# Kernel tuning notes

Hardware: AMD Instinct MI355X
Metric: run time of the kernel (lower is better)

The kernel has to match this reference:

```python
import jax, jax.numpy as jnp
import numpy as np

DIM = 1024
HEADS = 16
HEAD_DIM = DIM // HEADS
MLP_HIDDEN = DIM * 4
EPS = 1e-6


def _ln(x):
    # LayerNorm without affine, eps=1e-6
    mu = jnp.mean(x, axis=-1, keepdims=True)
    var = jnp.var(x, axis=-1, keepdims=True)
    return (x - mu) / jnp.sqrt(var + EPS)


def setup_inputs() -> dict:
    key = jax.random.key(0)
    ks = jax.random.split(key, 12)
    B, N = 8, 1024
    s = lambda fan: 1.0 / np.sqrt(fan)
    return {
        "x": jax.random.normal(ks[0], (B, N, DIM), jnp.float32),
        "c": jax.random.normal(ks[1], (B, DIM), jnp.float32),
        "w_qkv": jax.random.normal(ks[2], (DIM, 3 * DIM), jnp.float32) * s(DIM),
        "b_qkv": jnp.zeros((3 * DIM,), jnp.float32),
        "w_proj": jax.random.normal(ks[3], (DIM, DIM), jnp.float32) * s(DIM),
        "b_proj": jnp.zeros((DIM,), jnp.float32),
        "w_mlp1": jax.random.normal(ks[4], (DIM, MLP_HIDDEN), jnp.float32) * s(DIM),
        "b_mlp1": jnp.zeros((MLP_HIDDEN,), jnp.float32),
        "w_mlp2": jax.random.normal(ks[5], (MLP_HIDDEN, DIM), jnp.float32) * s(MLP_HIDDEN),
        "b_mlp2": jnp.zeros((DIM,), jnp.float32),
        "w_ada": jax.random.normal(ks[6], (DIM, 6 * DIM), jnp.float32) * s(DIM),
        "b_ada": jnp.zeros((6 * DIM,), jnp.float32),
    }


def _attention(h, w_qkv, b_qkv, w_proj, b_proj):
    B, N, C = h.shape
    qkv = h @ w_qkv + b_qkv  # [B,N,3C]
    qkv = qkv.reshape(B, N, 3, HEADS, HEAD_DIM)
    q, k, v = qkv[:, :, 0], qkv[:, :, 1], qkv[:, :, 2]  # [B,N,H,Dh]
    scale = HEAD_DIM ** -0.5
    attn = jnp.einsum("bqhd,bkhd->bhqk", q, k) * scale
    attn = jax.nn.softmax(attn, axis=-1)
    o = jnp.einsum("bhqk,bkhd->bqhd", attn, v).reshape(B, N, C)
    return o @ w_proj + b_proj


def reference(x, c, w_qkv, b_qkv, w_proj, b_proj, w_mlp1, b_mlp1, w_mlp2, b_mlp2, w_ada, b_ada):
    mod = (jax.nn.silu(c) @ w_ada + b_ada)[:, None, :]  # [B,1,6D]
    g1, be1, a1, g2, be2, a2 = jnp.split(mod, 6, axis=-1)
    h = _ln(x) * (1.0 + g1) + be1
    x = x + a1 * _attention(h, w_qkv, b_qkv, w_proj, b_proj)
    h = _ln(x) * (1.0 + g2) + be2
    mlp = jax.nn.gelu(h @ w_mlp1 + b_mlp1, approximate=False) @ w_mlp2 + b_mlp2
    return x + a2 * mlp
```

## Files before the change

kernel.cpp:

```cpp
#include <hip/hip_runtime.h>
#include <hip/hip_bf16.h>

#define DIMC 1024
#define SEQ  1024
#define NB   8
#define NH   16
#define HD2  64
#define EPSV 1e-6f

typedef short short8 __attribute__((ext_vector_type(8)));
typedef float floatx4 __attribute__((ext_vector_type(4)));

#define GLOAD_LDS(g, l) \
  __builtin_amdgcn_global_load_lds((const __attribute__((address_space(1))) unsigned int*)(g), \
                                   (__attribute__((address_space(3))) unsigned int*)(l), 16, 0, 0)

__device__ __forceinline__ float bf2f(unsigned short u){
  union { float f; unsigned int i; } v; v.i = ((unsigned int)u) << 16; return v.f;
}
__device__ __forceinline__ unsigned short f2bf(float f){
  union { float f; unsigned int i; } v; v.f = f;
  unsigned int r = v.i + 0x7fffu + ((v.i >> 16) & 1u);
  return (unsigned short)(r >> 16);
}

__device__ __forceinline__ float gelu_f(float v){
  const float z  = fabsf(v) * 0.70710678f;
  const float t  = __builtin_amdgcn_rcpf(fmaf(0.3275911f, z, 1.0f));
  float p = fmaf(t, 1.061405429f, -1.453152027f);
  p = fmaf(t, p, 1.421413741f);
  p = fmaf(t, p, -0.284496736f);
  p = fmaf(t, p, 0.254829592f);
  float erfz = fmaf(-p * t, __expf(-z * z), 1.0f);
  erfz = (v < 0.0f) ? -erfz : erfz;
  return 0.5f * v * (1.0f + erfz);
}

__global__ __launch_bounds__(256)
void tcvt_kernel(const float* __restrict__ in, unsigned short* __restrict__ out, int K, int N)
{
  __shared__ float tile[32][33];
  const int n0 = blockIdx.x * 32;
  const int k0 = blockIdx.y * 32;
  const int tx = threadIdx.x & 31;
  const int ty = threadIdx.x >> 5;
#pragma unroll
  for (int i = 0; i < 4; i++)
    tile[ty + i*8][tx] = in[(size_t)(k0 + ty + i*8) * N + n0 + tx];
  __syncthreads();
#pragma unroll
  for (int i = 0; i < 4; i++)
    out[(size_t)(n0 + ty + i*8) * K + k0 + tx] = f2bf(tile[tx][ty + i*8]);
}

__global__ __launch_bounds__(256)
void ada1_kernel(const float* __restrict__ c,
                 const float* __restrict__ w_ada,
                 float* __restrict__ partial)
{
  __shared__ float cs[NB][128];
  const int chunk = blockIdx.y;
  const int col = blockIdx.x * 256 + threadIdx.x;
  const int t = threadIdx.x;
  for (int i = t; i < NB * 128; i += 256) {
    const int b = i >> 7, k = i & 127;
    const float v = c[b * DIMC + chunk * 128 + k];
    cs[b][k] = v / (1.0f + __expf(-v));
  }
  __syncthreads();
  float acc[NB];
#pragma unroll
  for (int b = 0; b < NB; b++) acc[b] = 0.0f;
#pragma unroll 8
  for (int k = 0; k < 128; k++) {
    const float wv = w_ada[(size_t)(chunk * 128 + k) * 6144 + col];
#pragma unroll
    for (int b = 0; b < NB; b++) acc[b] = fmaf(cs[b][k], wv, acc[b]);
  }
#pragma unroll
  for (int b = 0; b < NB; b++)
    partial[((size_t)chunk * NB + b) * 6144 + col] = acc[b];
}

__global__ __launch_bounds__(256)
void ada2_kernel(const float* __restrict__ partial, const float* __restrict__ b_ada,
                 float* __restrict__ mod)
{
  const int i = blockIdx.x * 256 + threadIdx.x;
  const int b = i / 6144, col = i % 6144;
  float s = b_ada[col];
#pragma unroll
  for (int ch = 0; ch < 8; ch++) s += partial[((size_t)ch * NB + b) * 6144 + col];
  mod[i] = s;
}

__global__ __launch_bounds__(256)
void ln_kernel(const float* __restrict__ xin, const float* __restrict__ mod,
               int goff, int boff, unsigned short* __restrict__ hout)
{
  const int row = blockIdx.x;
  const int bb = row >> 10;
  const int t = threadIdx.x;
  const float4 x4 = *((const float4*)(xin + (size_t)row * DIMC) + t);
  const float v0 = x4.x, v1 = x4.y, v2 = x4.z, v3 = x4.w;
  float s  = v0 + v1 + v2 + v3;
  float ss = v0*v0 + v1*v1 + v2*v2 + v3*v3;
#pragma unroll
  for (int off = 32; off > 0; off >>= 1) {
    s  += __shfl_down(s,  off, 64);
    ss += __shfl_down(ss, off, 64);
  }
  __shared__ float red[10];
  const int w = t >> 6;
  if ((t & 63) == 0) { red[w] = s; red[4 + w] = ss; }
  __syncthreads();
  if (t == 0) {
    const float S  = red[0] + red[1] + red[2] + red[3];
    const float SS = red[4] + red[5] + red[6] + red[7];
    const float mu = S * (1.0f / 1024.0f);
    red[8] = mu;
    red[9] = rsqrtf(SS * (1.0f / 1024.0f) - mu * mu + EPSV);
  }
  __syncthreads();
  const float mu = red[8], rstd = red[9];
  const float* mrow = mod + (size_t)bb * 6144;
  const int d = t * 4;
  const float h0 = (v0 - mu) * rstd * (1.0f + mrow[goff + d + 0]) + mrow[boff + d + 0];
  const float h1 = (v1 - mu) * rstd * (1.0f + mrow[goff + d + 1]) + mrow[boff + d + 1];
  const float h2 = (v2 - mu) * rstd * (1.0f + mrow[goff + d + 2]) + mrow[boff + d + 2];
  const float h3 = (v3 - mu) * rstd * (1.0f + mrow[goff + d + 3]) + mrow[boff + d + 3];
  uint2 u;
  u.x = (unsigned)f2bf(h0) | ((unsigned)f2bf(h1) << 16);
  u.y = (unsigned)f2bf(h2) | ((unsigned)f2bf(h3) << 16);
  *((uint2*)(hout + (size_t)row * DIMC + d)) = u;
}

#define MF(a, b, c) __builtin_amdgcn_mfma_f32_16x16x32_bf16(a, b, c, 0, 0, 0)
#define FENCE() asm volatile("" ::: "memory")
#define BARRIER() do { FENCE(); __builtin_amdgcn_s_barrier(); FENCE(); } while (0)

template<int MODE, int BN>
__global__ __launch_bounds__(512, 2)
void gemm256_kernel(const unsigned short* __restrict__ A,
                    const unsigned short* __restrict__ Bt,
                    const float* __restrict__ bias,
                    void* __restrict__ Cout,
                    const float* __restrict__ resid,
                    const float* __restrict__ mod,
                    int M, int N, int K)
{
  constexpr int NWN = BN / 64;
  constexpr int NWM = 8 / NWN;
  constexpr int NI  = 256 / NWM / 16;

  __shared__ unsigned short As[2][16384];
  __shared__ unsigned short Bs[2][BN * 64];

  const int mT = M >> 8;
  const int mb = mT >> 3;
  const int bid = blockIdx.x;
  const int xcd = bid & 7;
  const int local = bid >> 3;
  const int ni = local / mb;
  const int mi = xcd * mb + (local - ni * mb);
  const int m0 = mi << 8, n0 = ni * BN;

  const int tid = threadIdx.x;
  const int w = tid >> 6, lane = tid & 63;
  const int quad = lane >> 4, c16 = lane & 15;
  const int wm = w / NWN, wn = w % NWN, w2 = w << 1;

  const int aRow = (wm * (NI * 16) + c16) * 64;
  const int bRow = (wn * 64 + c16) * 64;
  const int sxz  = (c16 & 7) << 4;
  const int swz0 = ((0  + quad * 16) ^ sxz) >> 1;
  const int swz1 = ((64 + quad * 16) ^ sxz) >> 1;
#define LDA8(cc, i, SW) (*(const short8*)&As[cc][aRow + (i) * 1024 + (SW)])
#define LDB8(cc, j, SW) (*(const short8*)&Bs[cc][bRow + (j) * 1024 + (SW)])

  const int l8 = lane >> 3, lc = lane & 7;
  const int stC = ((lc ^ l8) << 3);
  const unsigned short* aSt = A  + (size_t)(m0 + w2 * 8 + l8) * K + stC;
  const unsigned short* bSt = Bt + (size_t)(n0 + w2 * 8 + l8) * K + stC;
#define STAGE_A(cc, h, kk0) do { \
  GLOAD_LDS(aSt + (size_t)((h) * 128    ) * K + (kk0), &As[cc][(h) * 8192 + w2 * 512      ]); \
  GLOAD_LDS(aSt + (size_t)((h) * 128 + 8) * K + (kk0), &As[cc][(h) * 8192 + w2 * 512 + 512]); \
} while (0)
#define STAGE_B(cc, h, kk0) do { \
  GLOAD_LDS(bSt + (size_t)((h) * 128    ) * K + (kk0), &Bs[cc][(h) * 8192 + w2 * 512      ]); \
  GLOAD_LDS(bSt + (size_t)((h) * 128 + 8) * K + (kk0), &Bs[cc][(h) * 8192 + w2 * 512 + 512]); \
} while (0)

  floatx4 acc[NI][4];
#pragma unroll
  for (int i = 0; i < NI; i++)
#pragma unroll
    for (int j = 0; j < 4; j++) acc[i][j] = (floatx4)(0.0f);

#define MMROW(i, aE, aO) do { \
  acc[i][0] = MF(aE, bF00, acc[i][0]); acc[i][0] = MF(aO, bF01, acc[i][0]); \
  acc[i][1] = MF(aE, bF10, acc[i][1]); acc[i][1] = MF(aO, bF11, acc[i][1]); \
  acc[i][2] = MF(aE, bF20, acc[i][2]); acc[i][2] = MF(aO, bF21, acc[i][2]); \
  acc[i][3] = MF(aE, bF30, acc[i][3]); acc[i][3] = MF(aO, bF31, acc[i][3]); \
} while (0)

#define PH_TAIL(i0, i1) do { \
  BARRIER(); \
  asm volatile("s_waitcnt lgkmcnt(0)" ::: "memory"); \
  __builtin_amdgcn_s_setprio(1); \
  MMROW(i0, a0, a1); \
  MMROW(i1, a2, a3); \
  __builtin_amdgcn_s_setprio(0); \
} while (0)

#define GROUP256(cc, oo, g) do { \
  const int kA_ = ((g) + 1) << 6; const int kB_ = ((g) + 2) << 6; \
  const bool dA_ = kA_ < K; const bool dB_ = kB_ < K; \
  short8 bF00 = LDB8(cc, 0, swz0), bF01 = LDB8(cc, 0, swz1); \
  short8 bF10 = LDB8(cc, 1, swz0), bF11 = LDB8(cc, 1, swz1); \
  short8 bF20 = LDB8(cc, 2, swz0), bF21 = LDB8(cc, 2, swz1); \
  short8 bF30 = LDB8(cc, 3, swz0), bF31 = LDB8(cc, 3, swz1); \
  short8 a0 = LDA8(cc, 0, swz0), a1 = LDA8(cc, 0, swz1); \
  short8 a2 = LDA8(cc, 1, swz0), a3 = LDA8(cc, 1, swz1); \
  if (dA_) STAGE_A(oo, 0, kA_); \
  PH_TAIL(0, 1); \
  BARRIER(); \
  a0 = LDA8(cc, 2, swz0); a1 = LDA8(cc, 2, swz1); \
  a2 = LDA8(cc, 3, swz0); a3 = LDA8(cc, 3, swz1); \
  if (dA_) STAGE_A(oo, 1, kA_); \
  PH_TAIL(2, 3); \
  BARRIER(); \
  a0 = LDA8(cc, 4, swz0); a1 = LDA8(cc, 4, swz1); \
  a2 = LDA8(cc, 5, swz0); a3 = LDA8(cc, 5, swz1); \
  if (dB_) STAGE_B(cc, 0, kB_); \
  PH_TAIL(4, 5); \
  BARRIER(); \
  a0 = LDA8(cc, 6, swz0); a1 = LDA8(cc, 6, swz1); \
  a2 = LDA8(cc, 7, swz0); a3 = LDA8(cc, 7, swz1); \
  if (dB_) STAGE_B(cc, 1, kB_); \
  PH_TAIL(6, 7); \
  if (dB_) { asm volatile("s_waitcnt vmcnt(4)" ::: "memory"); } \
  else     { asm volatile("s_waitcnt vmcnt(0)" ::: "memory"); } \
  BARRIER(); \
} while (0)

#define GROUP128(cc, oo, g) do { \
  const int kA_ = ((g) + 1) << 6; const int kB_ = ((g) + 2) << 6; \
  const bool dA_ = kA_ < K; const bool dB_ = kB_ < K; \
  short8 bF00 = LDB8(cc, 0, swz0), bF01 = LDB8(cc, 0, swz1); \
  short8 bF10 = LDB8(cc, 1, swz0), bF11 = LDB8(cc, 1, swz1); \
  short8 bF20 = LDB8(cc, 2, swz0), bF21 = LDB8(cc, 2, swz1); \
  short8 bF30 = LDB8(cc, 3, swz0), bF31 = LDB8(cc, 3, swz1); \
  short8 a0 = LDA8(cc, 0, swz0), a1 = LDA8(cc, 0, swz1); \
  short8 a2 = LDA8(cc, 1, swz0), a3 = LDA8(cc, 1, swz1); \
  if (dA_) { STAGE_A(oo, 0, kA_); STAGE_A(oo, 1, kA_); } \
  PH_TAIL(0, 1); \
  BARRIER(); \
  a0 = LDA8(cc, 2, swz0); a1 = LDA8(cc, 2, swz1); \
  a2 = LDA8(cc, 3, swz0); a3 = LDA8(cc, 3, swz1); \
  if (dB_) STAGE_B(cc, 0, kB_); \
  PH_TAIL(2, 3); \
  if (dB_) { asm volatile("s_waitcnt vmcnt(2)" ::: "memory"); } \
  else     { asm volatile("s_waitcnt vmcnt(0)" ::: "memory"); } \
  BARRIER(); \
} while (0)

  if constexpr (BN == 256) {
    STAGE_B(0, 0, 0);  STAGE_B(0, 1, 0);
    STAGE_A(0, 0, 0);  STAGE_A(0, 1, 0);
    STAGE_B(1, 0, 64); STAGE_B(1, 1, 64);
    asm volatile("s_waitcnt vmcnt(4)" ::: "memory");
  } else {
    STAGE_B(0, 0, 0);
    STAGE_A(0, 0, 0);  STAGE_A(0, 1, 0);
    STAGE_B(1, 0, 64);
    asm volatile("s_waitcnt vmcnt(2)" ::: "memory");
  }
  BARRIER();

  const int T = K >> 6;
  for (int g = 0; g < T; g += 2) {
    if constexpr (BN == 256) { GROUP256(0, 1, g); GROUP256(1, 0, g + 1); }
    else                     { GROUP128(0, 1, g); GROUP128(1, 0, g + 1); }
  }

  const int bb = m0 >> 10;
  if (MODE == 0 || MODE == 1) {
    unsigned short* eb;
    if constexpr (BN == 256)
      eb = (w < 4 ? (unsigned short*)As : (unsigned short*)Bs) + (w & 3) * 8192;
    else
      eb = (unsigned short*)As + w * (NI * 1024);
#pragma unroll
    for (int j = 0; j < 4; j++) {
      const int col = n0 + wn * 64 + j * 16 + c16;
      const float bv = bias[col];
#pragma unroll
      for (int i = 0; i < NI; i++)
#pragma unroll
        for (int r = 0; r < 4; r++) {
          float v = acc[i][j][r] + bv;
          if (MODE == 1) v = gelu_f(v);
          eb[(i * 16 + quad * 4 + r) * 64 + j * 16 + c16] = f2bf(v);
        }
    }
    unsigned short* cw = (unsigned short*)Cout
                       + (size_t)(m0 + wm * (NI * 16)) * N + n0 + wn * 64;
    const int seg = lane & 7;
#pragma unroll
    for (int it = 0; it < NI * 2; it++) {
      const int row = it * 8 + (lane >> 3);
      *(uint4*)(cw + (size_t)row * N + seg * 8) = *(const uint4*)&eb[row * 64 + seg * 8];
    }
  } else {
#pragma unroll
    for (int j = 0; j < 4; j++) {
      const int col = n0 + wn * 64 + j * 16 + c16;
      const float bv = bias[col];
      const float av = mod[(size_t)bb * 6144 + (MODE == 2 ? 2048 : 5120) + col];
#pragma unroll
      for (int i = 0; i < NI; i++) {
        const int rowb = m0 + wm * (NI * 16) + i * 16 + quad * 4;
#pragma unroll
        for (int r = 0; r < 4; r++) {
          const size_t idx = (size_t)(rowb + r) * N + col;
          ((float*)Cout)[idx] = fmaf(av, acc[i][j][r] + bv, resid[idx]);
        }
      }
    }
  }
#undef GROUP256
#undef GROUP128
#undef PH_TAIL
#undef MMROW
#undef STAGE_A
#undef STAGE_B
#undef LDA8
#undef LDB8
}

__global__ __launch_bounds__(256, 2)
void fattn_kernel(const unsigned short* __restrict__ qkv, unsigned short* __restrict__ o_out)
{
  __shared__ unsigned short Ks[64][72];
  __shared__ unsigned short Vt[64][72];
  __shared__ unsigned short Pt[4][32][72];

  const int blk = blockIdx.x;
  const int qt = blk & 7;
  const int h  = (blk >> 3) & 15;
  const int bb = blk >> 7;
  const int tid = threadIdx.x;
  const int w = tid >> 6;
  const int lane = tid & 63;
  const int quad = lane >> 4;
  const int c16 = lane & 15;
  const int q0 = qt * 128 + w * 32;

  short8 qf[2][2];
#pragma unroll
  for (int msub = 0; msub < 2; msub++)
#pragma unroll
    for (int kh = 0; kh < 2; kh++) {
      const size_t idx = ((size_t)((bb*SEQ + q0 + msub*16 + c16) * 3 + 0)) * DIMC
                       + h * HD2 + kh * 32 + quad * 8;
      const uint4 u = *(const uint4*)(qkv + idx);
      const unsigned short* pu = (const unsigned short*)&u;
      short8 r;
#pragma unroll
      for (int j = 0; j < 8; j++) r[j] = (short)f2bf(bf2f(pu[j]) * 0.125f);
      qf[msub][kh] = r;
    }

  floatx4 oacc[2][4];
  float lsum[2][4];
#pragma unroll
  for (int msub = 0; msub < 2; msub++) {
#pragma unroll
    for (int r = 0; r < 4; r++) lsum[msub][r] = 0.0f;
#pragma unroll
    for (int d = 0; d < 4; d++) oacc[msub][d] = (floatx4)(0.0f);
  }

  const int tok = tid & 63;
  const int dg = tid >> 6;

  for (int kt = 0; kt < 16; kt++) {
    __syncthreads();
    {
      const size_t base = ((size_t)((bb*SEQ + kt*64 + tok) * 3)) * DIMC + h * HD2 + dg * 16;
      const uint4 ku0 = *(const uint4*)(qkv + base + DIMC);
      const uint4 ku1 = *(const uint4*)(qkv + base + DIMC + 8);
      const uint4 vu0 = *(const uint4*)(qkv + base + 2*DIMC);
      const uint4 vu1 = *(const uint4*)(qkv + base + 2*DIMC + 8);
      *(uint4*)&Ks[tok][dg*16]     = ku0;
      *(uint4*)&Ks[tok][dg*16 + 8] = ku1;
      const unsigned short* vp0 = (const unsigned short*)&vu0;
      const unsigned short* vp1 = (const unsigned short*)&vu1;
#pragma unroll
      for (int j = 0; j < 8; j++) Vt[dg*16 + j][tok] = vp0[j];
#pragma unroll
      for (int j = 0; j < 8; j++) Vt[dg*16 + 8 + j][tok] = vp1[j];
    }
    __syncthreads();

    floatx4 s[2][4];
#pragma unroll
    for (int msub = 0; msub < 2; msub++)
#pragma unroll
      for (int nsub = 0; nsub < 4; nsub++) s[msub][nsub] = (floatx4)(0.0f);
#pragma unroll
    for (int nsub = 0; nsub < 4; nsub++) {
      const short8 kf0 = *(const short8*)&Ks[nsub*16 + c16][quad*8];
      const short8 kf1 = *(const short8*)&Ks[nsub*16 + c16][32 + quad*8];
#pragma unroll
      for (int msub = 0; msub < 2; msub++) {
        s[msub][nsub] = __builtin_amdgcn_mfma_f32_16x16x32_bf16(qf[msub][0], kf0, s[msub][nsub], 0, 0, 0);
        s[msub][nsub] = __builtin_amdgcn_mfma_f32_16x16x32_bf16(qf[msub][1], kf1, s[msub][nsub], 0, 0, 0);
      }
    }

#pragma unroll
    for (int msub = 0; msub < 2; msub++)
#pragma unroll
      for (int nsub = 0; nsub < 4; nsub++)
#pragma unroll
        for (int r = 0; r < 4; r++) {
          const float p = __expf(s[msub][nsub][r] - 8.0f);
          lsum[msub][r] += p;
          Pt[w][msub*16 + quad*4 + r][nsub*16 + c16] = f2bf(p);
        }

    short8 pa[2][2];
#pragma unroll
    for (int msub = 0; msub < 2; msub++) {
      pa[msub][0] = *(const short8*)&Pt[w][msub*16 + c16][quad*8];
      pa[msub][1] = *(const short8*)&Pt[w][msub*16 + c16][32 + quad*8];
    }
#pragma unroll
    for (int dsub = 0; dsub < 4; dsub++) {
      const short8 vf0 = *(const short8*)&Vt[dsub*16 + c16][quad*8];
      const short8 vf1 = *(const short8*)&Vt[dsub*16 + c16][32 + quad*8];
#pragma unroll
      for (int msub = 0; msub < 2; msub++) {
        oacc[msub][dsub] = __builtin_amdgcn_mfma_f32_16x16x32_bf16(pa[msub][0], vf0, oacc[msub][dsub], 0, 0, 0);
        oacc[msub][dsub] = __builtin_amdgcn_mfma_f32_16x16x32_bf16(pa[msub][1], vf1, oacc[msub][dsub], 0, 0, 0);
      }
    }
  }

#pragma unroll
  for (int msub = 0; msub < 2; msub++) {
    float rl[4];
#pragma unroll
    for (int r = 0; r < 4; r++) {
      float t = lsum[msub][r];
#pragma unroll
      for (int xm = 1; xm < 16; xm <<= 1) t += __shfl_xor(t, xm, 64);
      rl[r] = 1.0f / t;
    }
#pragma unroll
    for (int dsub = 0; dsub < 4; dsub++)
#pragma unroll
      for (int r = 0; r < 4; r++) {
        const size_t idx = (size_t)(bb*SEQ + q0 + msub*16 + quad*4 + r) * DIMC
                         + h * HD2 + dsub*16 + c16;
        o_out[idx] = f2bf(oacc[msub][dsub][r] * rl[r]);
      }
  }
}

extern "C" void kernel_launch(void* const* d_in, const int* in_sizes, int n_in,
                              void* d_out, int out_size, void* d_ws, size_t ws_size,
                              hipStream_t stream) {
  const float* x      = (const float*)d_in[0];
  const float* c      = (const float*)d_in[1];
  const float* w_qkv  = (const float*)d_in[2];
  const float* b_qkv  = (const float*)d_in[3];
  const float* w_proj = (const float*)d_in[4];
  const float* b_proj = (const float*)d_in[5];
  const float* w_mlp1 = (const float*)d_in[6];
  const float* b_mlp1 = (const float*)d_in[7];
  const float* w_mlp2 = (const float*)d_in[8];
  const float* b_mlp2 = (const float*)d_in[9];
  const float* w_ada  = (const float*)d_in[10];
  const float* b_ada  = (const float*)d_in[11];

  char* ws = (char*)d_ws;
  float*          mod     = (float*)(ws);
  unsigned short* wqkv_t  = (unsigned short*)(ws + 196608);
  unsigned short* wproj_t = (unsigned short*)(ws + 6488064);
  unsigned short* wmlp1_t = (unsigned short*)(ws + 8585216);
  unsigned short* wmlp2_t = (unsigned short*)(ws + 16973824);
  unsigned short* bufH    = (unsigned short*)(ws + 25362432);
  float*          adapart = (float*)(ws + 25362432);
  unsigned short* qkv     = (unsigned short*)(ws + 42139648);
  unsigned short* hid     = (unsigned short*)(ws + 42139648);
  float*          out     = (float*)d_out;

  const int M = NB * SEQ;

  tcvt_kernel<<<dim3(96, 32),  256, 0, stream>>>(w_qkv,  wqkv_t,  1024, 3072);
  tcvt_kernel<<<dim3(32, 32),  256, 0, stream>>>(w_proj, wproj_t, 1024, 1024);
  tcvt_kernel<<<dim3(128, 32), 256, 0, stream>>>(w_mlp1, wmlp1_t, 1024, 4096);
  tcvt_kernel<<<dim3(32, 128), 256, 0, stream>>>(w_mlp2, wmlp2_t, 4096, 1024);

  ada1_kernel<<<dim3(24, 8), 256, 0, stream>>>(c, w_ada, adapart);
  ada2_kernel<<<192, 256, 0, stream>>>(adapart, b_ada, mod);

  ln_kernel<<<M, 256, 0, stream>>>(x, mod, 0, 1024, bufH);
  gemm256_kernel<0,128><<<768, 512, 0, stream>>>(bufH, wqkv_t, b_qkv, qkv, nullptr, nullptr, M, 3072, 1024);
  fattn_kernel<<<1024, 256, 0, stream>>>(qkv, bufH);
  gemm256_kernel<2,128><<<256, 512, 0, stream>>>(bufH, wproj_t, b_proj, out, x, mod, M, 1024, 1024);
  ln_kernel<<<M, 256, 0, stream>>>(out, mod, 3072, 4096, bufH);

  const size_t fullHidEnd = 42139648ull + (size_t)M * 4096 * 2;
  if (ws_size >= fullHidEnd) {
    gemm256_kernel<1,256><<<512, 512, 0, stream>>>(bufH, wmlp1_t, b_mlp1, hid,
                                                   nullptr, nullptr, M, 4096, 1024);
    gemm256_kernel<3,128><<<256, 512, 0, stream>>>(hid, wmlp2_t, b_mlp2, out,
                                                   out, mod, M, 1024, 4096);
  } else {
    for (int half = 0; half < 2; half++) {
      const size_t roff = (size_t)half * 4096;
      gemm256_kernel<1,256><<<256, 512, 0, stream>>>(bufH + roff * DIMC, wmlp1_t, b_mlp1, hid,
                                                     nullptr, nullptr, 4096, 4096, 1024);
      gemm256_kernel<3,128><<<128, 512, 0, stream>>>(hid, wmlp2_t, b_mlp2, out + roff * DIMC,
                                                     out + roff * DIMC, mod + (size_t)half * 4 * 6144,
                                                     4096, 1024, 4096);
    }
  }
}
```

Before: 494.1 us.

## Fuse weight prep kernels, generalize GEMM tile shape, swizzle epilogue staging

Merges the four weight transpose-convert launches and the ada partial GEMM into one prep kernel to cut launch overhead. Templates the GEMM on BM as well as BN, and switches the MLP2 GEMM to a 128x256 tile. Adds an XOR swizzle to the LDS epilogue staging buffer to reduce bank conflicts, and a sched_barrier before the MFMA phase. The mixed-branch prep kernel may lose some occupancy, and the new MLP2 tile shape changes per-block reuse and the grid mapping.

```diff
diff --git a/kernel.cpp b/kernel.cpp
--- a/kernel.cpp
+++ b/kernel.cpp
@@ -36,50 +36,69 @@
   return 0.5f * v * (1.0f + erfz);
 }
 
+__device__ __forceinline__ void tcvt_body(const float* __restrict__ in,
+                                          unsigned short* __restrict__ out,
+                                          int K, int N, int bx, int by, int t,
+                                          float* shbuf)
+{
+  const int n0 = bx * 32;
+  const int k0 = by * 32;
+  const int tx = t & 31;
+  const int ty = t >> 5;
+#pragma unroll
+  for (int i = 0; i < 4; i++)
+    shbuf[(ty + i*8) * 33 + tx] = in[(size_t)(k0 + ty + i*8) * N + n0 + tx];
+  __syncthreads();
+#pragma unroll
+  for (int i = 0; i < 4; i++)
+    out[(size_t)(n0 + ty + i*8) * K + k0 + tx] = f2bf(shbuf[tx * 33 + ty + i*8]);
+}
+
 __global__ __launch_bounds__(256)
-void tcvt_kernel(const float* __restrict__ in, unsigned short* __restrict__ out, int K, int N)
-{
-  __shared__ float tile[32][33];
-  const int n0 = blockIdx.x * 32;
-  const int k0 = blockIdx.y * 32;
-  const int tx = threadIdx.x & 31;
-  const int ty = threadIdx.x >> 5;
-#pragma unroll
-  for (int i = 0; i < 4; i++)
-    tile[ty + i*8][tx] = in[(size_t)(k0 + ty + i*8) * N + n0 + tx];
-  __syncthreads();
-#pragma unroll
-  for (int i = 0; i < 4; i++)
-    out[(size_t)(n0 + ty + i*8) * K + k0 + tx] = f2bf(tile[tx][ty + i*8]);
-}
-
-__global__ __launch_bounds__(256)
-void ada1_kernel(const float* __restrict__ c,
-                 const float* __restrict__ w_ada,
+void prep_kernel(const float* __restrict__ w_qkv,  unsigned short* __restrict__ wqkv_t,
+                 const float* __restrict__ w_proj, unsigned short* __restrict__ wproj_t,
+                 const float* __restrict__ w_mlp1, unsigned short* __restrict__ wmlp1_t,
+                 const float* __restrict__ w_mlp2, unsigned short* __restrict__ wmlp2_t,
+                 const float* __restrict__ c,      const float* __restrict__ w_ada,
                  float* __restrict__ partial)
 {
-  __shared__ float cs[NB][128];
-  const int chunk = blockIdx.y;
-  const int col = blockIdx.x * 256 + threadIdx.x;
+  __shared__ float shbuf[1056];
+  const int b = blockIdx.x;
   const int t = threadIdx.x;
-  for (int i = t; i < NB * 128; i += 256) {
-    const int b = i >> 7, k = i & 127;
-    const float v = c[b * DIMC + chunk * 128 + k];
-    cs[b][k] = v / (1.0f + __expf(-v));
-  }
-  __syncthreads();
-  float acc[NB];
-#pragma unroll
-  for (int b = 0; b < NB; b++) acc[b] = 0.0f;
+  if (b < 3072) {
+    tcvt_body(w_qkv, wqkv_t, 1024, 3072, b % 96, b / 96, t, shbuf);
+  } else if (b < 4096) {
+    const int r = b - 3072;
+    tcvt_body(w_proj, wproj_t, 1024, 1024, r % 32, r / 32, t, shbuf);
+  } else if (b < 8192) {
+    const int r = b - 4096;
+    tcvt_body(w_mlp1, wmlp1_t, 1024, 4096, r % 128, r / 128, t, shbuf);
+  } else if (b < 12288) {
+    const int r = b - 8192;
+    tcvt_body(w_mlp2, wmlp2_t, 4096, 1024, r % 32, r / 32, t, shbuf);
+  } else {
+    const int r = b - 12288;
+    const int chunk = r / 24;
+    const int col = (r % 24) * 256 + t;
+    for (int i = t; i < NB * 128; i += 256) {
+      const int bb = i >> 7, k = i & 127;
+      const float v = c[bb * DIMC + chunk * 128 + k];
+      shbuf[bb * 128 + k] = v / (1.0f + __expf(-v));
+    }
+    __syncthreads();
+    float acc[NB];
+#pragma unroll
+    for (int bb = 0; bb < NB; bb++) acc[bb] = 0.0f;
 #pragma unroll 8
-  for (int k = 0; k < 128; k++) {
-    const float wv = w_ada[(size_t)(chunk * 128 + k) * 6144 + col];
-#pragma unroll
-    for (int b = 0; b < NB; b++) acc[b] = fmaf(cs[b][k], wv, acc[b]);
-  }
-#pragma unroll
-  for (int b = 0; b < NB; b++)
-    partial[((size_t)chunk * NB + b) * 6144 + col] = acc[b];
+    for (int k = 0; k < 128; k++) {
+      const float wv = w_ada[(size_t)(chunk * 128 + k) * 6144 + col];
+#pragma unroll
+      for (int bb = 0; bb < NB; bb++) acc[bb] = fmaf(shbuf[bb * 128 + k], wv, acc[bb]);
+    }
+#pragma unroll
+    for (int bb = 0; bb < NB; bb++)
+      partial[((size_t)chunk * NB + bb) * 6144 + col] = acc[bb];
+  }
 }
 
 __global__ __launch_bounds__(256)
@@ -139,7 +158,7 @@
 #define FENCE() asm volatile("" ::: "memory")
 #define BARRIER() do { FENCE(); __builtin_amdgcn_s_barrier(); FENCE(); } while (0)
 
-template<int MODE, int BN>
+template<int MODE, int BM, int BN>
 __global__ __launch_bounds__(512, 2)
 void gemm256_kernel(const unsigned short* __restrict__ A,
                     const unsigned short* __restrict__ Bt,
@@ -151,24 +170,26 @@
 {
   constexpr int NWN = BN / 64;
   constexpr int NWM = 8 / NWN;
-  constexpr int NI  = 256 / NWM / 16;
-
-  __shared__ unsigned short As[2][16384];
+  constexpr int NI  = BM / NWM / 16;
+  constexpr int AU  = BM / 128;
+  constexpr int BU  = BN / 128;
+
+  __shared__ unsigned short As[2][BM * 64];
   __shared__ unsigned short Bs[2][BN * 64];
 
-  const int mT = M >> 8;
+  const int mT = M / BM;
   const int mb = mT >> 3;
   const int bid = blockIdx.x;
   const int xcd = bid & 7;
   const int local = bid >> 3;
   const int ni = local / mb;
   const int mi = xcd * mb + (local - ni * mb);
-  const int m0 = mi << 8, n0 = ni * BN;
+  const int m0 = mi * BM, n0 = ni * BN;
 
   const int tid = threadIdx.x;
   const int w = tid >> 6, lane = tid & 63;
   const int quad = lane >> 4, c16 = lane & 15;
-  const int wm = w / NWN, wn = w % NWN, w2 = w << 1;
+  const int wm = w / NWN, wn = w % NWN;
 
   const int aRow = (wm * (NI * 16) + c16) * 64;
   const int bRow = (wn * 64 + c16) * 64;
@@ -180,15 +201,21 @@
 
   const int l8 = lane >> 3, lc = lane & 7;
   const int stC = ((lc ^ l8) << 3);
-  const unsigned short* aSt = A  + (size_t)(m0 + w2 * 8 + l8) * K + stC;
-  const unsigned short* bSt = Bt + (size_t)(n0 + w2 * 8 + l8) * K + stC;
+  const int wRowA = w * (BM / 16);
+  const int wRowB = w * (BN / 16);
+  const unsigned short* aSt = A  + (size_t)(m0 + wRowA + l8) * K + stC;
+  const unsigned short* bSt = Bt + (size_t)(n0 + wRowB + l8) * K + stC;
 #define STAGE_A(cc, h, kk0) do { \
-  GLOAD_LDS(aSt + (size_t)((h) * 128    ) * K + (kk0), &As[cc][(h) * 8192 + w2 * 512      ]); \
-  GLOAD_LDS(aSt + (size_t)((h) * 128 + 8) * K + (kk0), &As[cc][(h) * 8192 + w2 * 512 + 512]); \
+  _Pragma("unroll") \
+  for (int u_ = 0; u_ < AU; u_++) \
+    GLOAD_LDS(aSt + (size_t)((h) * (BM/2) + u_*8) * K + (kk0), \
+              &As[cc][((h) * (BM/2) + u_*8 + wRowA) * 64]); \
 } while (0)
 #define STAGE_B(cc, h, kk0) do { \
-  GLOAD_LDS(bSt + (size_t)((h) * 128    ) * K + (kk0), &Bs[cc][(h) * 8192 + w2 * 512      ]); \
-  GLOAD_LDS(bSt + (size_t)((h) * 128 + 8) * K + (kk0), &Bs[cc][(h) * 8192 + w2 * 512 + 512]); \
+  _Pragma("unroll") \
+  for (int u_ = 0; u_ < BU; u_++) \
+    GLOAD_LDS(bSt + (size_t)((h) * (BN/2) + u_*8) * K + (kk0), \
+              &Bs[cc][((h) * (BN/2) + u_*8 + wRowB) * 64]); \
 } while (0)
 
   floatx4 acc[NI][4];
@@ -207,13 +234,20 @@
 #define PH_TAIL(i0, i1) do { \
   BARRIER(); \
   asm volatile("s_waitcnt lgkmcnt(0)" ::: "memory"); \
+  __builtin_amdgcn_sched_barrier(0); \
   __builtin_amdgcn_s_setprio(1); \
   MMROW(i0, a0, a1); \
   MMROW(i1, a2, a3); \
   __builtin_amdgcn_s_setprio(0); \
 } while (0)
 
-#define GROUP256(cc, oo, g) do { \
+#define VMCNT_TAIL(dB_) do { \
+  if (dB_) { if constexpr (BU == 1) { asm volatile("s_waitcnt vmcnt(2)" ::: "memory"); } \
+             else                   { asm volatile("s_waitcnt vmcnt(4)" ::: "memory"); } } \
+  else { asm volatile("s_waitcnt vmcnt(0)" ::: "memory"); } \
+} while (0)
+
+#define GROUP4(cc, oo, g) do { \
   const int kA_ = ((g) + 1) << 6; const int kB_ = ((g) + 2) << 6; \
   const bool dA_ = kA_ < K; const bool dB_ = kB_ < K; \
   short8 bF00 = LDB8(cc, 0, swz0), bF01 = LDB8(cc, 0, swz1); \
@@ -239,12 +273,11 @@
   a2 = LDA8(cc, 7, swz0); a3 = LDA8(cc, 7, swz1); \
   if (dB_) STAGE_B(cc, 1, kB_); \
   PH_TAIL(6, 7); \
-  if (dB_) { asm volatile("s_waitcnt vmcnt(4)" ::: "memory"); } \
-  else     { asm volatile("s_waitcnt vmcnt(0)" ::: "memory"); } \
-  BARRIER(); \
-} while (0)
-
-#define GROUP128(cc, oo, g) do { \
+  VMCNT_TAIL(dB_); \
+  BARRIER(); \
+} while (0)
+
+#define GROUP2(cc, oo, g) do { \
   const int kA_ = ((g) + 1) << 6; const int kB_ = ((g) + 2) << 6; \
   const bool dA_ = kA_ < K; const bool dB_ = kB_ < K; \
   short8 bF00 = LDB8(cc, 0, swz0), bF01 = LDB8(cc, 0, swz1); \
@@ -258,39 +291,32 @@
   BARRIER(); \
   a0 = LDA8(cc, 2, swz0); a1 = LDA8(cc, 2, swz1); \
   a2 = LDA8(cc, 3, swz0); a3 = LDA8(cc, 3, swz1); \
-  if (dB_) STAGE_B(cc, 0, kB_); \
+  if (dB_) { STAGE_B(cc, 0, kB_); STAGE_B(cc, 1, kB_); } \
   PH_TAIL(2, 3); \
-  if (dB_) { asm volatile("s_waitcnt vmcnt(2)" ::: "memory"); } \
-  else     { asm volatile("s_waitcnt vmcnt(0)" ::: "memory"); } \
-  BARRIER(); \
-} while (0)
-
-  if constexpr (BN == 256) {
-    STAGE_B(0, 0, 0);  STAGE_B(0, 1, 0);
-    STAGE_A(0, 0, 0);  STAGE_A(0, 1, 0);
-    STAGE_B(1, 0, 64); STAGE_B(1, 1, 64);
-    asm volatile("s_waitcnt vmcnt(4)" ::: "memory");
-  } else {
-    STAGE_B(0, 0, 0);
-    STAGE_A(0, 0, 0);  STAGE_A(0, 1, 0);
-    STAGE_B(1, 0, 64);
-    asm volatile("s_waitcnt vmcnt(2)" ::: "memory");
-  }
+  VMCNT_TAIL(dB_); \
+  BARRIER(); \
+} while (0)
+
+  STAGE_B(0, 0, 0);  STAGE_B(0, 1, 0);
+  STAGE_A(0, 0, 0);  STAGE_A(0, 1, 0);
+  STAGE_B(1, 0, 64); STAGE_B(1, 1, 64);
+  if constexpr (BU == 1) { asm volatile("s_waitcnt vmcnt(2)" ::: "memory"); }
+  else                   { asm volatile("s_waitcnt vmcnt(4)" ::: "memory"); }
   BARRIER();
 
   const int T = K >> 6;
   for (int g = 0; g < T; g += 2) {
-    if constexpr (BN == 256) { GROUP256(0, 1, g); GROUP256(1, 0, g + 1); }
-    else                     { GROUP128(0, 1, g); GROUP128(1, 0, g + 1); }
+    if constexpr (BM == 256 && BN == 256) { GROUP4(0, 1, g); GROUP4(1, 0, g + 1); }
+    else                                  { GROUP2(0, 1, g); GROUP2(1, 0, g + 1); }
   }
 
   const int bb = m0 >> 10;
   if (MODE == 0 || MODE == 1) {
-    unsigned short* eb;
-    if constexpr (BN == 256)
-      eb = (w < 4 ? (unsigned short*)As : (unsigned short*)Bs) + (w & 3) * 8192;
-    else
-      eb = (unsigned short*)As + w * (NI * 1024);
+    constexpr int EPW = NI * 1024;
+    constexpr int WIA = (2 * BM * 64) / EPW;
+    unsigned short* eb = (w < WIA)
+        ? (unsigned short*)As + w * EPW
+        : (unsigned short*)Bs + (w - WIA) * EPW;
 #pragma unroll
     for (int j = 0; j < 4; j++) {
       const int col = n0 + wn * 64 + j * 16 + c16;
@@ -301,7 +327,9 @@
         for (int r = 0; r < 4; r++) {
           float v = acc[i][j][r] + bv;
           if (MODE == 1) v = gelu_f(v);
-          eb[(i * 16 + quad * 4 + r) * 64 + j * 16 + c16] = f2bf(v);
+          const int row = i * 16 + quad * 4 + r;
+          const int pc8 = (j * 2 + (c16 >> 3)) ^ (row & 7);
+          eb[row * 64 + pc8 * 8 + (c16 & 7)] = f2bf(v);
         }
     }
     unsigned short* cw = (unsigned short*)Cout
@@ -310,7 +338,8 @@
 #pragma unroll
     for (int it = 0; it < NI * 2; it++) {
       const int row = it * 8 + (lane >> 3);
-      *(uint4*)(cw + (size_t)row * N + seg * 8) = *(const uint4*)&eb[row * 64 + seg * 8];
+      *(uint4*)(cw + (size_t)row * N + seg * 8) =
+          *(const uint4*)&eb[row * 64 + ((seg ^ (row & 7)) * 8)];
     }
   } else {
 #pragma unroll
@@ -329,9 +358,10 @@
       }
     }
   }
-#undef GROUP256
-#undef GROUP128
+#undef GROUP4
+#undef GROUP2
 #undef PH_TAIL
+#undef VMCNT_TAIL
 #undef MMROW
 #undef STAGE_A
 #undef STAGE_B
@@ -500,34 +530,31 @@
 
   const int M = NB * SEQ;
 
-  tcvt_kernel<<<dim3(96, 32),  256, 0, stream>>>(w_qkv,  wqkv_t,  1024, 3072);
-  tcvt_kernel<<<dim3(32, 32),  256, 0, stream>>>(w_proj, wproj_t, 1024, 1024);
-  tcvt_kernel<<<dim3(128, 32), 256, 0, stream>>>(w_mlp1, wmlp1_t, 1024, 4096);
-  tcvt_kernel<<<dim3(32, 128), 256, 0, stream>>>(w_mlp2, wmlp2_t, 4096, 1024);
-
-  ada1_kernel<<<dim3(24, 8), 256, 0, stream>>>(c, w_ada, adapart);
+  prep_kernel<<<12480, 256, 0, stream>>>(w_qkv, wqkv_t, w_proj, wproj_t,
+                                         w_mlp1, wmlp1_t, w_mlp2, wmlp2_t,
+                                         c, w_ada, adapart);
   ada2_kernel<<<192, 256, 0, stream>>>(adapart, b_ada, mod);
 
   ln_kernel<<<M, 256, 0, stream>>>(x, mod, 0, 1024, bufH);
-  gemm256_kernel<0,128><<<768, 512, 0, stream>>>(bufH, wqkv_t, b_qkv, qkv, nullptr, nullptr, M, 3072, 1024);
+  gemm256_kernel<0,256,128><<<768, 512, 0, stream>>>(bufH, wqkv_t, b_qkv, qkv, nullptr, nullptr, M, 3072, 1024);
   fattn_kernel<<<1024, 256, 0, stream>>>(qkv, bufH);
-  gemm256_kernel<2,128><<<256, 512, 0, stream>>>(bufH, wproj_t, b_proj, out, x, mod, M, 1024, 1024);
+  gemm256_kernel<2,256,128><<<256, 512, 0, stream>>>(bufH, wproj_t, b_proj, out, x, mod, M, 1024, 1024);
   ln_kernel<<<M, 256, 0, stream>>>(out, mod, 3072, 4096, bufH);
 
   const size_t fullHidEnd = 42139648ull + (size_t)M * 4096 * 2;
   if (ws_size >= fullHidEnd) {
-    gemm256_kernel<1,256><<<512, 512, 0, stream>>>(bufH, wmlp1_t, b_mlp1, hid,
-                                                   nullptr, nullptr, M, 4096, 1024);
-    gemm256_kernel<3,128><<<256, 512, 0, stream>>>(hid, wmlp2_t, b_mlp2, out,
-                                                   out, mod, M, 1024, 4096);
+    gemm256_kernel<1,256,256><<<512, 512, 0, stream>>>(bufH, wmlp1_t, b_mlp1, hid,
+                                                       nullptr, nullptr, M, 4096, 1024);
+    gemm256_kernel<3,128,256><<<256, 512, 0, stream>>>(hid, wmlp2_t, b_mlp2, out,
+                                                       out, mod, M, 1024, 4096);
   } else {
     for (int half = 0; half < 2; half++) {
       const size_t roff = (size_t)half * 4096;
-      gemm256_kernel<1,256><<<256, 512, 0, stream>>>(bufH + roff * DIMC, wmlp1_t, b_mlp1, hid,
-                                                     nullptr, nullptr, 4096, 4096, 1024);
-      gemm256_kernel<3,128><<<128, 512, 0, stream>>>(hid, wmlp2_t, b_mlp2, out + roff * DIMC,
-                                                     out + roff * DIMC, mod + (size_t)half * 4 * 6144,
-                                                     4096, 1024, 4096);
-    }
-  }
-}
+      gemm256_kernel<1,256,256><<<256, 512, 0, stream>>>(bufH + roff * DIMC, wmlp1_t, b_mlp1, hid,
+                                                         nullptr, nullptr, 4096, 4096, 1024);
+      gemm256_kernel<3,128,256><<<128, 512, 0, stream>>>(hid, wmlp2_t, b_mlp2, out + roff * DIMC,
+                                                         out + roff * DIMC, mod + (size_t)half * 4 * 6144,
+                                                         4096, 1024, 4096);
+    }
+  }
+}
```

Result: faster. 482.3 us (-2.4%).
